# Kernel optimization log

Measured on AMD Instinct MI355X. Metric: run time of the kernel, lower is better.

## Reference

```python
import jax, jax.numpy as jnp
import numpy as np

E, H = 512, 8
D = E // H  # head_dim = 64
NEG = jnp.finfo(jnp.float32).min


def setup_inputs() -> dict:
    key = jax.random.key(0)
    ks = jax.random.split(key, 12)
    s = 0.02
    return {
        "image": jax.random.normal(ks[0], (16, 197, E), jnp.float32),
        "text": jax.random.normal(ks[1], (64, 30, E), jnp.float32),
        "text_mask": jax.random.randint(ks[2], (64, 29), 0, 2).astype(bool),
        "Wq": jax.random.normal(ks[3], (D, D), jnp.float32) * s,
        "Wk": jax.random.normal(ks[4], (D, D), jnp.float32) * s,
        "Wv": jax.random.normal(ks[5], (D, D), jnp.float32) * s,
        "W_out": jax.random.normal(ks[6], (E, E), jnp.float32) * s,
        "b_out": jnp.zeros((E,), jnp.float32),
        "Wtv": jax.random.normal(ks[7], (D, D), jnp.float32) * s,
        "W_out_text": jax.random.normal(ks[8], (E, E), jnp.float32) * s,
        "b_out_text": jnp.zeros((E,), jnp.float32),
    }


def reference(image, text, text_mask, Wq, Wk, Wv, W_out, b_out, Wtv, W_out_text, b_out_text):
    I, Q, _ = image.shape
    T, K, _ = text.shape
    img = image.reshape(I, Q, H, D)
    txt = text.reshape(T, K, H, D)
    # per-head linear projections (torch Linear: y = x @ W.T)
    q = img @ Wq.T            # [I,Q,H,D]
    k = txt @ Wk.T            # [T,K,H,D]
    v = txt @ Wv.T            # [T,K,H,D]
    # cross-batch bidirectional attention energy [I,T,H,Q,K]
    energy = jnp.einsum('tkhd,iqhd->ithqk', k, q)
    # cls_present: pad mask with True at front along K
    mask = jnp.pad(text_mask, ((0, 0), (1, 0)), constant_values=True)  # [T,K]
    energy = jnp.where(mask[None, :, None, None, :], energy, NEG)
    scaled = energy / jnp.sqrt(jnp.float32(E))
    attention = jax.nn.softmax(scaled, axis=-1)       # over k (i2t)
    text_attention = jax.nn.softmax(scaled, axis=-2)  # over q (t2i)
    # i2t branch: [I,T,Q,H,D] -> [I,T,Q,E]
    out = jnp.einsum('ithqk,tkhd->itqhd', attention, v).reshape(I, T, Q, E)
    out = out @ W_out.T + b_out
    out = out.mean(axis=2)  # mean pool over image tokens -> [I,T,E]
    # t2i branch: [I,T,K,H,D] -> [I,T,K,E]
    tv = img @ Wtv.T  # [I,Q,H,D]
    out_text = jnp.einsum('ithqk,iqhd->itkhd', text_attention, tv).reshape(I, T, K, E)
    out_text = out_text @ W_out_text.T + b_out_text
    out_text = out_text.mean(axis=2)  # mean pool over text tokens -> [I,T,E]
    return (out, out_text, attention, text_attention)
```

## Files before the change

### kernel.cpp

```cpp
#include <hip/hip_runtime.h>
#include <hip/hip_bf16.h>
#include <cstdint>

#define I_ 16
#define T_ 64
#define Q_ 197
#define K_ 30
#define H_ 8
#define D_ 64
#define E_ 512

typedef float f32x2 __attribute__((ext_vector_type(2)));
typedef float f32x4 __attribute__((ext_vector_type(4)));
typedef short bf16x8 __attribute__((ext_vector_type(8)));

static constexpr float INV_SQRT_E = 0.044194173824159216f;
static constexpr float C197 = 1.0f / 197.0f;
static constexpr int   QK = Q_ * K_;

#define OFF_QBF   0
#define OFF_KBF   806912
#define OFF_V     1298432
#define OFF_TV    2281472
#define OFF_ASUM  3895296
#define OFF_TASUM 4141056
#define OFF_PBF   5754880
#define OFF_WBF   6279168

__global__ __launch_bounds__(512) void proj_kernel(
    const float* __restrict__ image, const float* __restrict__ text,
    const float* __restrict__ Wq, const float* __restrict__ Wk,
    const float* __restrict__ Wv, const float* __restrict__ Wtv,
    const float* __restrict__ W_out, const float* __restrict__ W_out_text,
    float* __restrict__ ws)
{
  const int NQ4 = (I_ * Q_) / 4;
  const int NT4 = (T_ * K_) / 4;
  int bb = blockIdx.x;
  int tid = threadIdx.x;

  if (bb >= NQ4 + 2 * NT4 + NQ4) {
    int row0 = (bb - (NQ4 + 2 * NT4 + NQ4)) * 4;
    __hip_bfloat16* Wb = (__hip_bfloat16*)(ws + OFF_WBF);
    const float* src = (row0 < 512) ? (W_out + row0 * E_) : (W_out_text + (row0 - 512) * E_);
    #pragma unroll
    for (int rr = 0; rr < 4; ++rr)
      Wb[(size_t)(row0 + rr) * E_ + tid] = __float2bfloat16(src[rr * E_ + tid]);
    return;
  }

  const float* X; const float* W; int row0; int mode;
  if (bb < NQ4)             { X = image; W = Wq;  row0 = bb * 4;               mode = 0; }
  else if (bb < NQ4 + NT4)  { X = text;  W = Wk;  row0 = (bb - NQ4) * 4;       mode = 1; }
  else if (bb < NQ4 + 2*NT4){ X = text;  W = Wv;  row0 = (bb - NQ4 - NT4) * 4; mode = 2; }
  else                      { X = image; W = Wtv; row0 = (bb - NQ4 - 2*NT4)*4; mode = 3; }

  __shared__ float s_x[4][E_];
  __shared__ float s_w[D_][D_ + 1];
  for (int idx = tid; idx < D_ * D_; idx += 512) s_w[idx >> 6][idx & 63] = W[idx];
  #pragma unroll
  for (int rr = 0; rr < 4; ++rr) s_x[rr][tid] = X[(size_t)(row0 + rr) * E_ + tid];
  __syncthreads();

  int h = tid >> 6, dout = tid & 63;
  float a0 = 0.f, a1 = 0.f, a2 = 0.f, a3 = 0.f;
  #pragma unroll
  for (int d = 0; d < D_; ++d) {
    float w = s_w[dout][d];
    a0 = fmaf(s_x[0][h * 64 + d], w, a0);
    a1 = fmaf(s_x[1][h * 64 + d], w, a1);
    a2 = fmaf(s_x[2][h * 64 + d], w, a2);
    a3 = fmaf(s_x[3][h * 64 + d], w, a3);
  }
  if (mode <= 1) {
    __hip_bfloat16* Y = (__hip_bfloat16*)(ws + (mode == 0 ? OFF_QBF : OFF_KBF));
    Y[(size_t)(row0 + 0) * E_ + tid] = __float2bfloat16(a0);
    Y[(size_t)(row0 + 1) * E_ + tid] = __float2bfloat16(a1);
    Y[(size_t)(row0 + 2) * E_ + tid] = __float2bfloat16(a2);
    Y[(size_t)(row0 + 3) * E_ + tid] = __float2bfloat16(a3);
  } else {
    float* Y = ws + (mode == 2 ? OFF_V : OFF_TV);
    Y[(size_t)(row0 + 0) * E_ + tid] = a0;
    Y[(size_t)(row0 + 1) * E_ + tid] = a1;
    Y[(size_t)(row0 + 2) * E_ + tid] = a2;
    Y[(size_t)(row0 + 3) * E_ + tid] = a3;
  }
}

__global__ __launch_bounds__(256, 8) void attn_kernel(
    const __hip_bfloat16* __restrict__ qbf, const __hip_bfloat16* __restrict__ kbf,
    const int* __restrict__ text_mask,
    float* __restrict__ attn_out, float* __restrict__ tattn_out,
    float* __restrict__ A_sum, float* __restrict__ TA_sum)
{
  int b = blockIdx.x;
  int h = b & 7, t = (b >> 3) & 63, i = b >> 9;
  int tid = threadIdx.x;
  int w = tid >> 6, lane = tid & 63;
  int lr = lane & 15, lg = lane >> 4;

  __shared__ __hip_bfloat16 s_e[208 * 30];
  __shared__ float s_invrow[208];
  __shared__ float s_cd[4][32];
  __shared__ float s_ca[4][32];
  __shared__ float s_invd[32];
  __shared__ int   s_mask[32];

  if (tid < 32) s_mask[tid] = (tid == 0) ? 1 : (tid < K_ ? text_mask[t * (K_ - 1) + tid - 1] : 0);

  int m0 = (lr == 0) ? 1 : text_mask[t * (K_ - 1) + lr - 1];
  int m1 = (lr < 14) ? text_mask[t * (K_ - 1) + 15 + lr] : 0;

  const __hip_bfloat16* qb = qbf + ((size_t)(i * Q_) * H_ + h) * D_;
  const __hip_bfloat16* kb = kbf + ((size_t)(t * K_) * H_ + h) * D_;

  const bf16x8* bp0 = (const bf16x8*)(kb + (size_t)lr * (H_ * D_) + lg * 8);
  const bf16x8* bp1 = (const bf16x8*)(kb + (size_t)(16 + lr) * (H_ * D_) + lg * 8);
  bf16x8 b00 = bp0[0], b01 = bp0[4];
  bf16x8 b10 = bp1[0], b11 = bp1[4];

  float cd0 = 0.f, cd1 = 0.f, ca0 = 0.f, ca1 = 0.f;

  #pragma unroll
  for (int j = 0; j < 4; ++j) {
    int mt = w + 4 * j;
    if (mt < 13) {
      const bf16x8* ap = (const bf16x8*)(qb + (size_t)(mt * 16 + lr) * (H_ * D_) + lg * 8);
      bf16x8 a0 = ap[0], a1 = ap[4];
      f32x4 acc0 = {0.f, 0.f, 0.f, 0.f}, acc1 = {0.f, 0.f, 0.f, 0.f};
      acc0 = __builtin_amdgcn_mfma_f32_16x16x32_bf16(a0, b00, acc0, 0, 0, 0);
      acc0 = __builtin_amdgcn_mfma_f32_16x16x32_bf16(a1, b01, acc0, 0, 0, 0);
      acc1 = __builtin_amdgcn_mfma_f32_16x16x32_bf16(a0, b10, acc1, 0, 0, 0);
      acc1 = __builtin_amdgcn_mfma_f32_16x16x32_bf16(a1, b11, acc1, 0, 0, 0);
      int row0 = mt * 16 + lg * 4;
      float v0[4], v1[4];
      #pragma unroll
      for (int r = 0; r < 4; ++r) {
        bool vr = (row0 + r) < Q_;
        v0[r] = (vr && m0) ? __expf(acc0[r] * INV_SQRT_E) : 0.f;
        v1[r] = (vr && m1) ? __expf(acc1[r] * INV_SQRT_E) : 0.f;
        s_e[(row0 + r) * K_ + lr] = __float2bfloat16(v0[r]);
        if (lr < 14) s_e[(row0 + r) * K_ + 16 + lr] = __float2bfloat16(v1[r]);
      }
      #pragma unroll
      for (int r = 0; r < 4; ++r) {
        float s = v0[r] + v1[r];
        s += __shfl_xor(s, 1);
        s += __shfl_xor(s, 2);
        s += __shfl_xor(s, 4);
        s += __shfl_xor(s, 8);
        float iv = ((row0 + r) < Q_ && s > 0.f) ? (1.0f / s) : 0.f;
        if (lr == 0) s_invrow[row0 + r] = iv;
        cd0 += v0[r]; ca0 += v0[r] * iv;
        cd1 += v1[r]; ca1 += v1[r] * iv;
      }
    }
  }

  cd0 += __shfl_xor(cd0, 16); cd0 += __shfl_xor(cd0, 32);
  ca0 += __shfl_xor(ca0, 16); ca0 += __shfl_xor(ca0, 32);
  cd1 += __shfl_xor(cd1, 16); cd1 += __shfl_xor(cd1, 32);
  ca1 += __shfl_xor(ca1, 16); ca1 += __shfl_xor(ca1, 32);
  if (lane < 16) {
    s_cd[w][lr] = cd0; s_cd[w][lr + 16] = cd1;
    s_ca[w][lr] = ca0; s_ca[w][lr + 16] = ca1;
  }
  __syncthreads();

  if (tid < 32) {
    int col = tid;
    float d  = s_cd[0][col] + s_cd[1][col] + s_cd[2][col] + s_cd[3][col];
    float pa = s_ca[0][col] + s_ca[1][col] + s_ca[2][col] + s_ca[3][col];
    s_invd[col] = (s_mask[col] && d > 0.f) ? (1.0f / d) : 0.f;
    if (col < K_) A_sum[(size_t)b * K_ + col] = pa;
  }
  __syncthreads();

  if (tid < Q_) {
    float ta = 0.f;
    #pragma unroll
    for (int kk = 0; kk < K_; ++kk) {
      float ev = __bfloat162float(s_e[tid * K_ + kk]);
      ta += s_mask[kk] ? ev * s_invd[kk] : C197;
    }
    TA_sum[(size_t)b * Q_ + tid] = ta;
  }

  {
    float* abase = attn_out  + (size_t)b * QK;
    float* tbase = tattn_out + (size_t)b * QK;
    int head = (b & 1) ? 2 : 0;
    if (tid == 0) {
      int e0 = head ? 0 : (QK - 2);
      float ex = __bfloat162float(s_e[e0]);
      float ey = __bfloat162float(s_e[e0 + 1]);
      int r0 = e0 / K_, c0 = e0 - r0 * K_;
      int r1 = (e0 + 1) / K_, c1 = (e0 + 1) - r1 * K_;
      f32x2 av = { ex * s_invrow[r0], ey * s_invrow[r1] };
      f32x2 tv2 = { s_mask[c0] ? ex * s_invd[c0] : C197,
                    s_mask[c1] ? ey * s_invd[c1] : C197 };
      __builtin_nontemporal_store(av,  (f32x2*)(abase + e0));
      __builtin_nontemporal_store(tv2, (f32x2*)(tbase + e0));
    }
    for (int fi = tid; fi < 1477; fi += 256) {
      int base = head + fi * 4;
      float ev[4]; int rw[4]; int cl[4];
      #pragma unroll
      for (int e = 0; e < 4; ++e) {
        int idx = base + e;
        ev[e] = __bfloat162float(s_e[idx]);
        rw[e] = idx / K_;
        cl[e] = idx - rw[e] * K_;
      }
      f32x4 av, tv4;
      #pragma unroll
      for (int e = 0; e < 4; ++e) {
        av[e]  = ev[e] * s_invrow[rw[e]];
        tv4[e] = s_mask[cl[e]] ? ev[e] * s_invd[cl[e]] : C197;
      }
      __builtin_nontemporal_store(av,  (f32x4*)(abase + base));
      __builtin_nontemporal_store(tv4, (f32x4*)(tbase + base));
    }
  }
}

__global__ __launch_bounds__(512) void pool_fused_kernel(
    const float* __restrict__ A_sum, const float* __restrict__ TA_sum,
    const float* __restrict__ ws_v, const float* __restrict__ ws_tv,
    __hip_bfloat16* __restrict__ Pbf)
{
  int bt = blockIdx.x;
  int t = bt & 63;
  int i = bt >> 6;
  int tid = threadIdx.x;
  int h = tid >> 6, d = tid & 63;
  __shared__ float s_A[H_ * K_];
  __shared__ float s_TA[H_ * Q_];
  if (tid < H_ * K_) s_A[tid] = A_sum[(size_t)bt * H_ * K_ + tid];
  for (int idx = tid; idx < H_ * Q_; idx += 512) s_TA[idx] = TA_sum[(size_t)bt * H_ * Q_ + idx];
  __syncthreads();

  {
    float a0 = 0.f, a1 = 0.f;
    #pragma unroll
    for (int kk = 0; kk < K_; kk += 2) {
      a0 = fmaf(s_A[h * K_ + kk],     ws_v[((size_t)(t * K_ + kk)     * H_ + h) * D_ + d], a0);
      a1 = fmaf(s_A[h * K_ + kk + 1], ws_v[((size_t)(t * K_ + kk + 1) * H_ + h) * D_ + d], a1);
    }
    Pbf[(size_t)bt * E_ + tid] = __float2bfloat16((a0 + a1) * C197);
  }

  {
    float a0 = 0.f, a1 = 0.f, a2 = 0.f, a3 = 0.f;
    int qq = 0;
    for (; qq + 4 <= Q_; qq += 4) {
      a0 = fmaf(s_TA[h * Q_ + qq + 0], ws_tv[((size_t)(i * Q_ + qq + 0) * H_ + h) * D_ + d], a0);
      a1 = fmaf(s_TA[h * Q_ + qq + 1], ws_tv[((size_t)(i * Q_ + qq + 1) * H_ + h) * D_ + d], a1);
      a2 = fmaf(s_TA[h * Q_ + qq + 2], ws_tv[((size_t)(i * Q_ + qq + 2) * H_ + h) * D_ + d], a2);
      a3 = fmaf(s_TA[h * Q_ + qq + 3], ws_tv[((size_t)(i * Q_ + qq + 3) * H_ + h) * D_ + d], a3);
    }
    for (; qq < Q_; ++qq)
      a0 = fmaf(s_TA[h * Q_ + qq], ws_tv[((size_t)(i * Q_ + qq) * H_ + h) * D_ + d], a0);
    Pbf[(size_t)(1024 + bt) * E_ + tid] = __float2bfloat16(((a0 + a1) + (a2 + a3)) * (1.0f / 30.0f));
  }
}

__global__ __launch_bounds__(256) void outproj_mfma_kernel(
    const __hip_bfloat16* __restrict__ Pbf, const __hip_bfloat16* __restrict__ Wbf,
    const float* __restrict__ b_out, const float* __restrict__ b_out_text,
    float* __restrict__ out)
{
  int mt = blockIdx.x;
  int z = (mt >= 64);
  int tid = threadIdx.x;
  int w = tid >> 6, lane = tid & 63;
  int lr = lane & 15, lg = lane >> 4;

  const __hip_bfloat16* A = Pbf + (size_t)(mt * 16 + lr) * E_ + lg * 8;
  const __hip_bfloat16* B = Wbf + (size_t)(z * 512) * E_;
  f32x4 acc[8] = {};
  for (int ks = 0; ks < 16; ++ks) {
    bf16x8 a = *(const bf16x8*)(A + ks * 32);
    #pragma unroll
    for (int nt = 0; nt < 8; ++nt) {
      int n0 = w * 128 + nt * 16;
      bf16x8 bv = *(const bf16x8*)(B + (size_t)(n0 + lr) * E_ + ks * 32 + lg * 8);
      acc[nt] = __builtin_amdgcn_mfma_f32_16x16x32_bf16(a, bv, acc[nt], 0, 0, 0);
    }
  }
  const float* bias = z ? b_out_text : b_out;
  int row0 = mt * 16 + lg * 4;
  #pragma unroll
  for (int nt = 0; nt < 8; ++nt) {
    int n = w * 128 + nt * 16 + lr;
    float bv = bias[n];
    #pragma unroll
    for (int r = 0; r < 4; ++r)
      out[(size_t)(row0 + r) * E_ + n] = acc[nt][r] + bv;
  }
}

extern "C" void kernel_launch(void* const* d_in, const int* in_sizes, int n_in,
                              void* d_out, int out_size, void* d_ws, size_t ws_size,
                              hipStream_t stream)
{
  const float* image      = (const float*)d_in[0];
  const float* text       = (const float*)d_in[1];
  const int*   tmask      = (const int*)d_in[2];
  const float* Wq         = (const float*)d_in[3];
  const float* Wk         = (const float*)d_in[4];
  const float* Wv         = (const float*)d_in[5];
  const float* W_out      = (const float*)d_in[6];
  const float* b_out      = (const float*)d_in[7];
  const float* Wtv        = (const float*)d_in[8];
  const float* W_out_text = (const float*)d_in[9];
  const float* b_out_text = (const float*)d_in[10];

  float* out = (float*)d_out;
  float* ws  = (float*)d_ws;

  const __hip_bfloat16* qbf = (const __hip_bfloat16*)(ws + OFF_QBF);
  const __hip_bfloat16* kbf = (const __hip_bfloat16*)(ws + OFF_KBF);
  float* v     = ws + OFF_V;
  float* tv    = ws + OFF_TV;
  float* Asum  = ws + OFF_ASUM;
  float* TAsum = ws + OFF_TASUM;
  __hip_bfloat16* Pbf = (__hip_bfloat16*)(ws + OFF_PBF);
  __hip_bfloat16* Wbf = (__hip_bfloat16*)(ws + OFF_WBF);

  float* attn    = out + (size_t)2 * I_ * T_ * E_;
  float* tattn   = attn + (size_t)I_ * T_ * H_ * Q_ * K_;

  const int NQ4 = (I_ * Q_) / 4, NT4 = (T_ * K_) / 4;
  proj_kernel<<<NQ4 + 2 * NT4 + NQ4 + 256, 512, 0, stream>>>(
      image, text, Wq, Wk, Wv, Wtv, W_out, W_out_text, ws);
  attn_kernel<<<I_ * T_ * H_, 256, 0, stream>>>(qbf, kbf, tmask, attn, tattn, Asum, TAsum);
  pool_fused_kernel<<<I_ * T_, 512, 0, stream>>>(Asum, TAsum, v, tv, Pbf);
  outproj_mfma_kernel<<<128, 256, 0, stream>>>(Pbf, Wbf, b_out, b_out_text, out);
}
```

Measured before the change: 194.9 us.

## Fuse pooled attention-value reductions into the attention kernel

Removes the separate pool kernel. Each attention block now builds its own per-head attention column sums and text-attention row sums in shared memory and reduces them against V and TV, writing the pooled bf16 rows directly. This drops one kernel launch and the global round trip of the A_sum/TA_sum buffers. In exchange, the attention kernel gets extra shared memory, two more block barriers, and strided fp32 loads of V/TV from every block, which may lower occupancy.

```diff
diff --git a/kernel.cpp b/kernel.cpp
--- a/kernel.cpp
+++ b/kernel.cpp
@@ -22,8 +22,6 @@
 #define OFF_KBF   806912
 #define OFF_V     1298432
 #define OFF_TV    2281472
-#define OFF_ASUM  3895296
-#define OFF_TASUM 4141056
 #define OFF_PBF   5754880
 #define OFF_WBF   6279168
 
@@ -90,8 +88,9 @@
 __global__ __launch_bounds__(256, 8) void attn_kernel(
     const __hip_bfloat16* __restrict__ qbf, const __hip_bfloat16* __restrict__ kbf,
     const int* __restrict__ text_mask,
+    const float* __restrict__ ws_v, const float* __restrict__ ws_tv,
     float* __restrict__ attn_out, float* __restrict__ tattn_out,
-    float* __restrict__ A_sum, float* __restrict__ TA_sum)
+    __hip_bfloat16* __restrict__ Pbf)
 {
   int b = blockIdx.x;
   int h = b & 7, t = (b >> 3) & 63, i = b >> 9;
@@ -101,9 +100,11 @@
 
   __shared__ __hip_bfloat16 s_e[208 * 30];
   __shared__ float s_invrow[208];
-  __shared__ float s_cd[4][32];
-  __shared__ float s_ca[4][32];
+  __shared__ float s_cd[4][64];
+  __shared__ float s_ca[4][64];
   __shared__ float s_invd[32];
+  __shared__ float s_asum[32];
+  __shared__ float s_ta[208];
   __shared__ int   s_mask[32];
 
   if (tid < 32) s_mask[tid] = (tid == 0) ? 1 : (tid < K_ ? text_mask[t * (K_ - 1) + tid - 1] : 0);
@@ -172,9 +173,11 @@
     float d  = s_cd[0][col] + s_cd[1][col] + s_cd[2][col] + s_cd[3][col];
     float pa = s_ca[0][col] + s_ca[1][col] + s_ca[2][col] + s_ca[3][col];
     s_invd[col] = (s_mask[col] && d > 0.f) ? (1.0f / d) : 0.f;
-    if (col < K_) A_sum[(size_t)b * K_ + col] = pa;
-  }
-  __syncthreads();
+    s_asum[col] = pa;
+  }
+  __syncthreads();
+
+  int d = tid & 63, g = tid >> 6;
 
   if (tid < Q_) {
     float ta = 0.f;
@@ -183,9 +186,15 @@
       float ev = __bfloat162float(s_e[tid * K_ + kk]);
       ta += s_mask[kk] ? ev * s_invd[kk] : C197;
     }
-    TA_sum[(size_t)b * Q_ + tid] = ta;
-  }
-
+    s_ta[tid] = ta;
+  }
+  {
+    float p = 0.f;
+    int k0 = g * 8, k1 = (k0 + 8 < K_) ? (k0 + 8) : K_;
+    for (int kk = k0; kk < k1; ++kk)
+      p = fmaf(s_asum[kk], ws_v[((size_t)(t * K_ + kk) * H_ + h) * D_ + d], p);
+    s_cd[g][d] = p;
+  }
   {
     float* abase = attn_out  + (size_t)b * QK;
     float* tbase = tattn_out + (size_t)b * QK;
@@ -222,46 +231,24 @@
       __builtin_nontemporal_store(tv4, (f32x4*)(tbase + base));
     }
   }
-}
-
-__global__ __launch_bounds__(512) void pool_fused_kernel(
-    const float* __restrict__ A_sum, const float* __restrict__ TA_sum,
-    const float* __restrict__ ws_v, const float* __restrict__ ws_tv,
-    __hip_bfloat16* __restrict__ Pbf)
-{
-  int bt = blockIdx.x;
-  int t = bt & 63;
-  int i = bt >> 6;
-  int tid = threadIdx.x;
-  int h = tid >> 6, d = tid & 63;
-  __shared__ float s_A[H_ * K_];
-  __shared__ float s_TA[H_ * Q_];
-  if (tid < H_ * K_) s_A[tid] = A_sum[(size_t)bt * H_ * K_ + tid];
-  for (int idx = tid; idx < H_ * Q_; idx += 512) s_TA[idx] = TA_sum[(size_t)bt * H_ * Q_ + idx];
-  __syncthreads();
-
+  __syncthreads();
+
+  if (tid < 64) {
+    float s = (s_cd[0][tid] + s_cd[1][tid]) + (s_cd[2][tid] + s_cd[3][tid]);
+    Pbf[(size_t)(i * T_ + t) * E_ + h * 64 + tid] = __float2bfloat16(s * C197);
+  }
   {
-    float a0 = 0.f, a1 = 0.f;
-    #pragma unroll
-    for (int kk = 0; kk < K_; kk += 2) {
-      a0 = fmaf(s_A[h * K_ + kk],     ws_v[((size_t)(t * K_ + kk)     * H_ + h) * D_ + d], a0);
-      a1 = fmaf(s_A[h * K_ + kk + 1], ws_v[((size_t)(t * K_ + kk + 1) * H_ + h) * D_ + d], a1);
-    }
-    Pbf[(size_t)bt * E_ + tid] = __float2bfloat16((a0 + a1) * C197);
-  }
-
-  {
-    float a0 = 0.f, a1 = 0.f, a2 = 0.f, a3 = 0.f;
-    int qq = 0;
-    for (; qq + 4 <= Q_; qq += 4) {
-      a0 = fmaf(s_TA[h * Q_ + qq + 0], ws_tv[((size_t)(i * Q_ + qq + 0) * H_ + h) * D_ + d], a0);
-      a1 = fmaf(s_TA[h * Q_ + qq + 1], ws_tv[((size_t)(i * Q_ + qq + 1) * H_ + h) * D_ + d], a1);
-      a2 = fmaf(s_TA[h * Q_ + qq + 2], ws_tv[((size_t)(i * Q_ + qq + 2) * H_ + h) * D_ + d], a2);
-      a3 = fmaf(s_TA[h * Q_ + qq + 3], ws_tv[((size_t)(i * Q_ + qq + 3) * H_ + h) * D_ + d], a3);
-    }
-    for (; qq < Q_; ++qq)
-      a0 = fmaf(s_TA[h * Q_ + qq], ws_tv[((size_t)(i * Q_ + qq) * H_ + h) * D_ + d], a0);
-    Pbf[(size_t)(1024 + bt) * E_ + tid] = __float2bfloat16(((a0 + a1) + (a2 + a3)) * (1.0f / 30.0f));
+    float p = 0.f;
+    int q0 = g * 50, q1 = (q0 + 50 < Q_) ? (q0 + 50) : Q_;
+    for (int qq = q0; qq < q1; ++qq)
+      p = fmaf(s_ta[qq], ws_tv[((size_t)(i * Q_ + qq) * H_ + h) * D_ + d], p);
+    s_ca[g][d] = p;
+  }
+  __syncthreads();
+
+  if (tid < 64) {
+    float s = (s_ca[0][tid] + s_ca[1][tid]) + (s_ca[2][tid] + s_ca[3][tid]);
+    Pbf[(size_t)(1024 + i * T_ + t) * E_ + h * 64 + tid] = __float2bfloat16(s * (1.0f / 30.0f));
   }
 }
 
@@ -323,8 +310,6 @@
   const __hip_bfloat16* kbf = (const __hip_bfloat16*)(ws + OFF_KBF);
   float* v     = ws + OFF_V;
   float* tv    = ws + OFF_TV;
-  float* Asum  = ws + OFF_ASUM;
-  float* TAsum = ws + OFF_TASUM;
   __hip_bfloat16* Pbf = (__hip_bfloat16*)(ws + OFF_PBF);
   __hip_bfloat16* Wbf = (__hip_bfloat16*)(ws + OFF_WBF);
 
@@ -334,7 +319,6 @@
   const int NQ4 = (I_ * Q_) / 4, NT4 = (T_ * K_) / 4;
   proj_kernel<<<NQ4 + 2 * NT4 + NQ4 + 256, 512, 0, stream>>>(
       image, text, Wq, Wk, Wv, Wtv, W_out, W_out_text, ws);
-  attn_kernel<<<I_ * T_ * H_, 256, 0, stream>>>(qbf, kbf, tmask, attn, tattn, Asum, TAsum);
-  pool_fused_kernel<<<I_ * T_, 512, 0, stream>>>(Asum, TAsum, v, tv, Pbf);
+  attn_kernel<<<I_ * T_ * H_, 256, 0, stream>>>(qbf, kbf, tmask, v, tv, attn, tattn, Pbf);
   outproj_mfma_kernel<<<128, 256, 0, stream>>>(Pbf, Wbf, b_out, b_out_text, out);
 }
```

New measurement: 212.0 us. +8.8%, slower.

## Keep attention exponentials in registers by transposing MFMA operands, drop LDS staging

Applied to the files above, without the earlier changes.

Swaps the MFMA operand order so each lane holds four consecutive key columns for one query row. Row sums then need only two cross-lane shuffles, and the exponentials stay in registers (packed as bf16) instead of being staged in a shared-memory tile. Both attention outputs are written directly from registers as float2 nontemporal stores, replacing the LDS readback pass with its per-element integer division. The launch-bounds occupancy hint drops from 8 to 4 to make room for the extra registers, and stores are now narrower and less coalesced than the previous float4 streaming pass.

```diff
diff --git a/kernel.cpp b/kernel.cpp
--- a/kernel.cpp
+++ b/kernel.cpp
@@ -26,6 +26,9 @@
 #define OFF_TASUM 4141056
 #define OFF_PBF   5754880
 #define OFF_WBF   6279168
+
+__device__ inline short f2bs(float x) { __hip_bfloat16 h = __float2bfloat16(x); return *reinterpret_cast<short*>(&h); }
+__device__ inline float bs2f(short s) { __hip_bfloat16 h = *reinterpret_cast<__hip_bfloat16*>(&s); return __bfloat162float(h); }
 
 __global__ __launch_bounds__(512) void proj_kernel(
     const float* __restrict__ image, const float* __restrict__ text,
@@ -87,7 +90,7 @@
   }
 }
 
-__global__ __launch_bounds__(256, 8) void attn_kernel(
+__global__ __launch_bounds__(256, 4) void attn_kernel(
     const __hip_bfloat16* __restrict__ qbf, const __hip_bfloat16* __restrict__ kbf,
     const int* __restrict__ text_mask,
     float* __restrict__ attn_out, float* __restrict__ tattn_out,
@@ -99,127 +102,150 @@
   int w = tid >> 6, lane = tid & 63;
   int lr = lane & 15, lg = lane >> 4;
 
-  __shared__ __hip_bfloat16 s_e[208 * 30];
-  __shared__ float s_invrow[208];
   __shared__ float s_cd[4][32];
   __shared__ float s_ca[4][32];
   __shared__ float s_invd[32];
-  __shared__ int   s_mask[32];
-
-  if (tid < 32) s_mask[tid] = (tid == 0) ? 1 : (tid < K_ ? text_mask[t * (K_ - 1) + tid - 1] : 0);
-
-  int m0 = (lr == 0) ? 1 : text_mask[t * (K_ - 1) + lr - 1];
-  int m1 = (lr < 14) ? text_mask[t * (K_ - 1) + 15 + lr] : 0;
+
+  int mA[4], mB[4];
+  #pragma unroll
+  for (int r = 0; r < 4; ++r) {
+    int kA = 4 * lg + r;
+    mA[r] = (kA == 0) ? 1 : text_mask[t * (K_ - 1) + kA - 1];
+    int kB = 16 + 4 * lg + r;
+    mB[r] = (kB < K_) ? text_mask[t * (K_ - 1) + kB - 1] : 0;
+  }
 
   const __hip_bfloat16* qb = qbf + ((size_t)(i * Q_) * H_ + h) * D_;
   const __hip_bfloat16* kb = kbf + ((size_t)(t * K_) * H_ + h) * D_;
 
   const bf16x8* bp0 = (const bf16x8*)(kb + (size_t)lr * (H_ * D_) + lg * 8);
   const bf16x8* bp1 = (const bf16x8*)(kb + (size_t)(16 + lr) * (H_ * D_) + lg * 8);
-  bf16x8 b00 = bp0[0], b01 = bp0[4];
-  bf16x8 b10 = bp1[0], b11 = bp1[4];
-
-  float cd0 = 0.f, cd1 = 0.f, ca0 = 0.f, ca1 = 0.f;
+  bf16x8 kf00 = bp0[0], kf01 = bp0[4];
+  bf16x8 kf10 = bp1[0], kf11 = bp1[4];
+
+  float cdA[4] = {}, cdB[4] = {}, caA[4] = {}, caB[4] = {};
+  bf16x8 epk[4];
+
+  float* abase = attn_out + (size_t)b * QK;
 
   #pragma unroll
   for (int j = 0; j < 4; ++j) {
-    int mt = w + 4 * j;
-    if (mt < 13) {
-      const bf16x8* ap = (const bf16x8*)(qb + (size_t)(mt * 16 + lr) * (H_ * D_) + lg * 8);
-      bf16x8 a0 = ap[0], a1 = ap[4];
+    int qt = w + 4 * j;
+    epk[j] = bf16x8{0, 0, 0, 0, 0, 0, 0, 0};
+    if (qt < 13) {
+      int qrow = qt * 16 + lr;
+      const bf16x8* qp = (const bf16x8*)(qb + (size_t)qrow * (H_ * D_) + lg * 8);
+      bf16x8 q0 = qp[0], q1 = qp[4];
       f32x4 acc0 = {0.f, 0.f, 0.f, 0.f}, acc1 = {0.f, 0.f, 0.f, 0.f};
-      acc0 = __builtin_amdgcn_mfma_f32_16x16x32_bf16(a0, b00, acc0, 0, 0, 0);
-      acc0 = __builtin_amdgcn_mfma_f32_16x16x32_bf16(a1, b01, acc0, 0, 0, 0);
-      acc1 = __builtin_amdgcn_mfma_f32_16x16x32_bf16(a0, b10, acc1, 0, 0, 0);
-      acc1 = __builtin_amdgcn_mfma_f32_16x16x32_bf16(a1, b11, acc1, 0, 0, 0);
-      int row0 = mt * 16 + lg * 4;
-      float v0[4], v1[4];
+      acc0 = __builtin_amdgcn_mfma_f32_16x16x32_bf16(kf00, q0, acc0, 0, 0, 0);
+      acc0 = __builtin_amdgcn_mfma_f32_16x16x32_bf16(kf01, q1, acc0, 0, 0, 0);
+      acc1 = __builtin_amdgcn_mfma_f32_16x16x32_bf16(kf10, q0, acc1, 0, 0, 0);
+      acc1 = __builtin_amdgcn_mfma_f32_16x16x32_bf16(kf11, q1, acc1, 0, 0, 0);
+      bool vr = qrow < Q_;
+      float eA[4], eB[4];
       #pragma unroll
       for (int r = 0; r < 4; ++r) {
-        bool vr = (row0 + r) < Q_;
-        v0[r] = (vr && m0) ? __expf(acc0[r] * INV_SQRT_E) : 0.f;
-        v1[r] = (vr && m1) ? __expf(acc1[r] * INV_SQRT_E) : 0.f;
-        s_e[(row0 + r) * K_ + lr] = __float2bfloat16(v0[r]);
-        if (lr < 14) s_e[(row0 + r) * K_ + 16 + lr] = __float2bfloat16(v1[r]);
-      }
+        eA[r] = (vr && mA[r]) ? __expf(acc0[r] * INV_SQRT_E) : 0.f;
+        eB[r] = (vr && mB[r]) ? __expf(acc1[r] * INV_SQRT_E) : 0.f;
+      }
+      float rs = ((eA[0] + eA[1]) + (eA[2] + eA[3])) + ((eB[0] + eB[1]) + (eB[2] + eB[3]));
+      rs += __shfl_xor(rs, 16);
+      rs += __shfl_xor(rs, 32);
+      float ivr = (vr && rs > 0.f) ? (1.0f / rs) : 0.f;
       #pragma unroll
       for (int r = 0; r < 4; ++r) {
-        float s = v0[r] + v1[r];
-        s += __shfl_xor(s, 1);
-        s += __shfl_xor(s, 2);
-        s += __shfl_xor(s, 4);
-        s += __shfl_xor(s, 8);
-        float iv = ((row0 + r) < Q_ && s > 0.f) ? (1.0f / s) : 0.f;
-        if (lr == 0) s_invrow[row0 + r] = iv;
-        cd0 += v0[r]; ca0 += v0[r] * iv;
-        cd1 += v1[r]; ca1 += v1[r] * iv;
-      }
-    }
-  }
-
-  cd0 += __shfl_xor(cd0, 16); cd0 += __shfl_xor(cd0, 32);
-  ca0 += __shfl_xor(ca0, 16); ca0 += __shfl_xor(ca0, 32);
-  cd1 += __shfl_xor(cd1, 16); cd1 += __shfl_xor(cd1, 32);
-  ca1 += __shfl_xor(ca1, 16); ca1 += __shfl_xor(ca1, 32);
-  if (lane < 16) {
-    s_cd[w][lr] = cd0; s_cd[w][lr + 16] = cd1;
-    s_ca[w][lr] = ca0; s_ca[w][lr + 16] = ca1;
+        cdA[r] += eA[r]; caA[r] += eA[r] * ivr;
+        cdB[r] += eB[r]; caB[r] += eB[r] * ivr;
+      }
+      if (vr) {
+        float* arow = abase + qrow * K_;
+        f32x2 s0 = { eA[0] * ivr, eA[1] * ivr };
+        f32x2 s1 = { eA[2] * ivr, eA[3] * ivr };
+        __builtin_nontemporal_store(s0, (f32x2*)(arow + 4 * lg));
+        __builtin_nontemporal_store(s1, (f32x2*)(arow + 4 * lg + 2));
+        f32x2 s2 = { eB[0] * ivr, eB[1] * ivr };
+        __builtin_nontemporal_store(s2, (f32x2*)(arow + 16 + 4 * lg));
+        if (lg < 3) {
+          f32x2 s3 = { eB[2] * ivr, eB[3] * ivr };
+          __builtin_nontemporal_store(s3, (f32x2*)(arow + 16 + 4 * lg + 2));
+        }
+      }
+      epk[j] = bf16x8{ f2bs(eA[0]), f2bs(eA[1]), f2bs(eA[2]), f2bs(eA[3]),
+                       f2bs(eB[0]), f2bs(eB[1]), f2bs(eB[2]), f2bs(eB[3]) };
+    }
+  }
+
+  #pragma unroll
+  for (int r = 0; r < 4; ++r) {
+    cdA[r] += __shfl_xor(cdA[r], 1); cdA[r] += __shfl_xor(cdA[r], 2);
+    cdA[r] += __shfl_xor(cdA[r], 4); cdA[r] += __shfl_xor(cdA[r], 8);
+    cdB[r] += __shfl_xor(cdB[r], 1); cdB[r] += __shfl_xor(cdB[r], 2);
+    cdB[r] += __shfl_xor(cdB[r], 4); cdB[r] += __shfl_xor(cdB[r], 8);
+    caA[r] += __shfl_xor(caA[r], 1); caA[r] += __shfl_xor(caA[r], 2);
+    caA[r] += __shfl_xor(caA[r], 4); caA[r] += __shfl_xor(caA[r], 8);
+    caB[r] += __shfl_xor(caB[r], 1); caB[r] += __shfl_xor(caB[r], 2);
+    caB[r] += __shfl_xor(caB[r], 4); caB[r] += __shfl_xor(caB[r], 8);
+  }
+  if (lr == 0) {
+    #pragma unroll
+    for (int r = 0; r < 4; ++r) {
+      s_cd[w][4 * lg + r] = cdA[r];
+      s_ca[w][4 * lg + r] = caA[r];
+      s_cd[w][16 + 4 * lg + r] = cdB[r];
+      s_ca[w][16 + 4 * lg + r] = caB[r];
+    }
   }
   __syncthreads();
 
   if (tid < 32) {
-    int col = tid;
-    float d  = s_cd[0][col] + s_cd[1][col] + s_cd[2][col] + s_cd[3][col];
-    float pa = s_ca[0][col] + s_ca[1][col] + s_ca[2][col] + s_ca[3][col];
-    s_invd[col] = (s_mask[col] && d > 0.f) ? (1.0f / d) : 0.f;
-    if (col < K_) A_sum[(size_t)b * K_ + col] = pa;
+    float dsum = (s_cd[0][tid] + s_cd[1][tid]) + (s_cd[2][tid] + s_cd[3][tid]);
+    float pa   = (s_ca[0][tid] + s_ca[1][tid]) + (s_ca[2][tid] + s_ca[3][tid]);
+    int mc = (tid == 0) ? 1 : (tid < K_ ? text_mask[t * (K_ - 1) + tid - 1] : 0);
+    s_invd[tid] = (mc && dsum > 0.f) ? (1.0f / dsum) : 0.f;
+    if (tid < K_) A_sum[(size_t)b * K_ + tid] = pa;
   }
   __syncthreads();
 
-  if (tid < Q_) {
-    float ta = 0.f;
-    #pragma unroll
-    for (int kk = 0; kk < K_; ++kk) {
-      float ev = __bfloat162float(s_e[tid * K_ + kk]);
-      ta += s_mask[kk] ? ev * s_invd[kk] : C197;
-    }
-    TA_sum[(size_t)b * Q_ + tid] = ta;
-  }
-
-  {
-    float* abase = attn_out  + (size_t)b * QK;
-    float* tbase = tattn_out + (size_t)b * QK;
-    int head = (b & 1) ? 2 : 0;
-    if (tid == 0) {
-      int e0 = head ? 0 : (QK - 2);
-      float ex = __bfloat162float(s_e[e0]);
-      float ey = __bfloat162float(s_e[e0 + 1]);
-      int r0 = e0 / K_, c0 = e0 - r0 * K_;
-      int r1 = (e0 + 1) / K_, c1 = (e0 + 1) - r1 * K_;
-      f32x2 av = { ex * s_invrow[r0], ey * s_invrow[r1] };
-      f32x2 tv2 = { s_mask[c0] ? ex * s_invd[c0] : C197,
-                    s_mask[c1] ? ey * s_invd[c1] : C197 };
-      __builtin_nontemporal_store(av,  (f32x2*)(abase + e0));
-      __builtin_nontemporal_store(tv2, (f32x2*)(tbase + e0));
-    }
-    for (int fi = tid; fi < 1477; fi += 256) {
-      int base = head + fi * 4;
-      float ev[4]; int rw[4]; int cl[4];
+  float idA[4], idB[4];
+  #pragma unroll
+  for (int r = 0; r < 4; ++r) { idA[r] = s_invd[4 * lg + r]; idB[r] = s_invd[16 + 4 * lg + r]; }
+
+  float* tbase = tattn_out + (size_t)b * QK;
+  #pragma unroll
+  for (int j = 0; j < 4; ++j) {
+    int qt = w + 4 * j;
+    if (qt < 13) {
+      int qrow = qt * 16 + lr;
+      bool vr = qrow < Q_;
+      float tvA[4], tvB[4];
       #pragma unroll
-      for (int e = 0; e < 4; ++e) {
-        int idx = base + e;
-        ev[e] = __bfloat162float(s_e[idx]);
-        rw[e] = idx / K_;
-        cl[e] = idx - rw[e] * K_;
-      }
-      f32x4 av, tv4;
+      for (int r = 0; r < 4; ++r) {
+        float e = bs2f(epk[j][r]);
+        tvA[r] = mA[r] ? e * idA[r] : C197;
+      }
       #pragma unroll
-      for (int e = 0; e < 4; ++e) {
-        av[e]  = ev[e] * s_invrow[rw[e]];
-        tv4[e] = s_mask[cl[e]] ? ev[e] * s_invd[cl[e]] : C197;
-      }
-      __builtin_nontemporal_store(av,  (f32x4*)(abase + base));
-      __builtin_nontemporal_store(tv4, (f32x4*)(tbase + base));
+      for (int r = 0; r < 4; ++r) {
+        float e = bs2f(epk[j][4 + r]);
+        int kB = 16 + 4 * lg + r;
+        tvB[r] = (kB < K_) ? (mB[r] ? e * idB[r] : C197) : 0.f;
+      }
+      float ta = ((tvA[0] + tvA[1]) + (tvA[2] + tvA[3])) + ((tvB[0] + tvB[1]) + (tvB[2] + tvB[3]));
+      ta += __shfl_xor(ta, 16);
+      ta += __shfl_xor(ta, 32);
+      if (vr) {
+        float* trow = tbase + qrow * K_;
+        f32x2 s0 = { tvA[0], tvA[1] };
+        f32x2 s1 = { tvA[2], tvA[3] };
+        __builtin_nontemporal_store(s0, (f32x2*)(trow + 4 * lg));
+        __builtin_nontemporal_store(s1, (f32x2*)(trow + 4 * lg + 2));
+        f32x2 s2 = { tvB[0], tvB[1] };
+        __builtin_nontemporal_store(s2, (f32x2*)(trow + 16 + 4 * lg));
+        if (lg < 3) {
+          f32x2 s3 = { tvB[2], tvB[3] };
+          __builtin_nontemporal_store(s3, (f32x2*)(trow + 16 + 4 * lg + 2));
+        }
+        if (lg == 0) TA_sum[(size_t)b * Q_ + qrow] = ta;
+      }
     }
   }
 }
```

After: 363.4 us. 1.86x slower.
